# Performance work log

Measured on AMD Instinct MI355X. Metric: run time of the kernel, lower is better.

## Reference

```python
import jax, jax.numpy as jnp
import numpy as np

B, T, D = 2, 2048, 2048
H, KV, HD, RD = 16, 4, 128, 64  # n_heads, n_kv_heads, head_dim, rope_head_dim
THETA = 10000.0


def setup_inputs() -> dict:
    key = jax.random.key(0)
    ks = jax.random.split(key, 5)
    x = jax.random.normal(ks[0], (B, T, D), dtype=jnp.float32)
    Wq = jax.random.normal(ks[1], (D, H * HD), dtype=jnp.float32) * 0.02
    Wk = jax.random.normal(ks[2], (D, KV * HD), dtype=jnp.float32) * 0.02
    Wv = jax.random.normal(ks[3], (D, KV * HD), dtype=jnp.float32) * 0.02
    Wo = jax.random.normal(ks[4], (H * HD, D), dtype=jnp.float32) * 0.02
    # RoPE frequencies for the first RD dims of each head
    inv_freq = 1.0 / (THETA ** (jnp.arange(0, RD, 2, dtype=jnp.float32) / RD))  # [RD/2]
    ang = jnp.arange(T, dtype=jnp.float32)[:, None] * inv_freq[None, :]         # [T, RD/2]
    return {"x": x, "freqs_cos": jnp.cos(ang), "freqs_sin": jnp.sin(ang),
            "Wq": Wq, "Wk": Wk, "Wv": Wv, "Wo": Wo}


def _apply_rope(t, cos, sin):
    # t: [B, h, T, HD]; rotate first RD dims treating consecutive pairs as complex
    rot = t[..., :RD].reshape(*t.shape[:-1], RD // 2, 2)
    e, o = rot[..., 0], rot[..., 1]
    c = cos[None, None]  # [1,1,T,RD/2]
    s = sin[None, None]
    re = e * c - o * s
    ro = e * s + o * c
    rot_out = jnp.stack([re, ro], axis=-1).reshape(*t.shape[:-1], RD)
    return jnp.concatenate([rot_out, t[..., RD:]], axis=-1)


def reference(x, freqs_cos, freqs_sin, Wq, Wk, Wv, Wo):
    q = (x @ Wq).reshape(B, T, H, HD).transpose(0, 2, 1, 3)   # [B,H,T,HD]
    k = (x @ Wk).reshape(B, T, KV, HD).transpose(0, 2, 1, 3)  # [B,KV,T,HD]
    v = (x @ Wv).reshape(B, T, KV, HD).transpose(0, 2, 1, 3)
    q = _apply_rope(q, freqs_cos, freqs_sin)
    k = _apply_rope(k, freqs_cos, freqs_sin)
    present_k, present_v = k, v
    rep = H // KV
    kr = jnp.repeat(k, rep, axis=1)  # GQA repeat_interleave -> [B,H,T,HD]
    vr = jnp.repeat(v, rep, axis=1)
    scores = jnp.einsum('bhqd,bhkd->bhqk', q, kr) / jnp.sqrt(jnp.asarray(HD, q.dtype))
    causal = jnp.tril(jnp.ones((T, T), dtype=bool))
    scores = jnp.where(causal[None, None], scores, jnp.asarray(-1e9, scores.dtype))
    attn = jax.nn.softmax(scores, axis=-1)
    y = jnp.einsum('bhqk,bhkd->bhqd', attn, vr)
    y = y.transpose(0, 2, 1, 3).reshape(B, T, H * HD) @ Wo  # [B,T,D]
    return y, present_k, present_v
```

## Files before the change

kernel.cpp:

```cpp
#include <hip/hip_runtime.h>
#include <hip/hip_bf16.h>

static constexpr int B_  = 2;
static constexpr int T_  = 2048;
static constexpr int D_  = 2048;
static constexpr int H_  = 16;
static constexpr int KV_ = 4;
static constexpr int HD_ = 128;
static constexpr int RD_ = 64;
static constexpr int BT_ = B_ * T_;
static constexpr float SCALE_ = 0.08838834764831845f;

typedef __attribute__((ext_vector_type(8))) short bf16x8;
typedef __attribute__((ext_vector_type(8))) unsigned short u16x8;
typedef __attribute__((ext_vector_type(4))) float f32x4;

#define COMPILER_BARRIER() __asm__ __volatile__("" ::: "memory")

typedef const __attribute__((address_space(1))) unsigned int* as1_u32p;
typedef __attribute__((address_space(3))) unsigned int* as3_u32p;
#define GLOAD16(g, l) __builtin_amdgcn_global_load_lds((as1_u32p)(const void*)(g), (as3_u32p)(void*)(l), 16, 0, 0)

__device__ __forceinline__ unsigned short f2bu(float f) {
  unsigned x = __float_as_uint(f);
  unsigned r = (x + 0x7fffu + ((x >> 16) & 1u)) >> 16;
  return (unsigned short)r;
}

__global__ __launch_bounds__(256) void cvt_bf16(const float* __restrict__ in,
                                                unsigned short* __restrict__ out) {
  const size_t i = ((size_t)blockIdx.x * 256 + threadIdx.x) * 4;
  const float4 f = *(const float4*)(in + i);
  ushort4 o;
  o.x = f2bu(f.x); o.y = f2bu(f.y); o.z = f2bu(f.z); o.w = f2bu(f.w);
  *(ushort4*)(out + i) = o;
}

__global__ __launch_bounds__(256) void t32(const float* __restrict__ in,
                                           unsigned short* __restrict__ out,
                                           int R, int C) {
  __shared__ unsigned short tile[32][36];
  const int r0 = blockIdx.x * 32;
  const int c0 = blockIdx.y * 32;
  const int tid = threadIdx.x;
  {
    const int r = tid >> 3;
    const int c = (tid & 7) * 4;
    const float4 f = *(const float4*)(in + (size_t)(r0 + r) * C + c0 + c);
    ushort4 w;
    w.x = f2bu(f.x); w.y = f2bu(f.y); w.z = f2bu(f.z); w.w = f2bu(f.w);
    *(ushort4*)&tile[r][c] = w;
  }
  __syncthreads();
  {
    const int c = tid >> 3;
    const int r = (tid & 7) * 4;
    ushort4 o;
    o.x = tile[r + 0][c];
    o.y = tile[r + 1][c];
    o.z = tile[r + 2][c];
    o.w = tile[r + 3][c];
    *(ushort4*)(out + (size_t)(c0 + c) * R + r0 + r) = o;
  }
}

template <int REMAP>
__global__ __launch_bounds__(256) void gemm_bf16(const unsigned short* __restrict__ A,
                                                 const unsigned short* __restrict__ Bt,
                                                 float* __restrict__ C,
                                                 int M, int N, int K) {
  __shared__ __align__(16) unsigned short As[128 * 32];
  __shared__ __align__(16) unsigned short Bs[128 * 32];
  const int tid = threadIdx.x;
  const int lane = tid & 63;
  const int wave = tid >> 6;
  const int n16 = lane & 15;
  const int quad = lane >> 4;
  const int bm = blockIdx.y * 128;
  const int bn = blockIdx.x * 128;
  const int wm = (wave & 1) * 64;
  const int wn = (wave >> 1) * 64;

  const int gr = tid >> 2;
  const int gc = (tid & 3) * 8;
  const unsigned short* agA = A  + (size_t)(bm + gr) * K + gc;
  const unsigned short* agB = A  + (size_t)(bm + 64 + gr) * K + gc;
  const unsigned short* bgA = Bt + (size_t)(bn + gr) * K + gc;
  const unsigned short* bgB = Bt + (size_t)(bn + 64 + gr) * K + gc;
  unsigned short* lAs0 = As + wave * 512;
  unsigned short* lAs1 = As + 2048 + wave * 512;
  unsigned short* lBs0 = Bs + wave * 512;
  unsigned short* lBs1 = Bs + 2048 + wave * 512;

  f32x4 acc[4][4];
#pragma unroll
  for (int mi = 0; mi < 4; ++mi)
#pragma unroll
    for (int ni = 0; ni < 4; ++ni) acc[mi][ni] = (f32x4){0.f, 0.f, 0.f, 0.f};

  for (int k0 = 0; k0 < K; k0 += 32) {
    GLOAD16(agA + k0, lAs0);
    GLOAD16(agB + k0, lAs1);
    GLOAD16(bgA + k0, lBs0);
    GLOAD16(bgB + k0, lBs1);
    __syncthreads();

    bf16x8 af[4], bf[4];
#pragma unroll
    for (int i = 0; i < 4; ++i) {
      af[i] = *(const bf16x8*)&As[(wm + i * 16 + n16) * 32 + quad * 8];
      bf[i] = *(const bf16x8*)&Bs[(wn + i * 16 + n16) * 32 + quad * 8];
    }
#pragma unroll
    for (int mi = 0; mi < 4; ++mi)
#pragma unroll
      for (int ni = 0; ni < 4; ++ni)
        acc[mi][ni] = __builtin_amdgcn_mfma_f32_16x16x32_bf16(af[mi], bf[ni], acc[mi][ni], 0, 0, 0);
    __syncthreads();
  }

#pragma unroll
  for (int mi = 0; mi < 4; ++mi) {
#pragma unroll
    for (int r = 0; r < 4; ++r) {
      const int row = bm + wm + mi * 16 + quad * 4 + r;
#pragma unroll
      for (int ni = 0; ni < 4; ++ni) {
        const int col = bn + wn + ni * 16 + n16;
        const float v = acc[mi][ni][r];
        if (REMAP == 0) {
          C[(size_t)row * N + col] = v;
        } else {
          const int b = row >> 11, t = row & (T_ - 1);
          const int part = col >> 9;
          const int kv = (col >> 7) & 3;
          const int hd = col & 127;
          C[(size_t)part * (B_ * KV_ * T_ * HD_) +
            (((size_t)(b * KV_ + kv) * T_) + t) * HD_ + hd] = v;
        }
      }
    }
  }
}

__global__ __launch_bounds__(256) void rope_q(float* __restrict__ Q,
                                              const float* __restrict__ cosb,
                                              const float* __restrict__ sinb) {
  const int bt = blockIdx.x;
  const int t = bt % T_;
  const int tid = threadIdx.x;
  for (int i = tid; i < H_ * (RD_ / 2); i += 256) {
    const int h = i >> 5;
    const int p = i & 31;
    const float c = cosb[t * 32 + p];
    const float s = sinb[t * 32 + p];
    const size_t base = (size_t)bt * (H_ * HD_) + h * HD_ + 2 * p;
    const float e = Q[base], o = Q[base + 1];
    Q[base]     = e * c - o * s;
    Q[base + 1] = e * s + o * c;
  }
}

__global__ __launch_bounds__(256) void rope_k(float* __restrict__ kout,
                                              const float* __restrict__ cosb,
                                              const float* __restrict__ sinb,
                                              unsigned short* __restrict__ Kbf) {
  const int bt = blockIdx.x;
  const int t = bt % T_;
  const int b = bt / T_;
  const int tid = threadIdx.x;
  for (int i = tid; i < KV_ * (HD_ / 2); i += 256) {
    const int kv = i >> 6;
    const int p = i & 63;
    const size_t idx = (((size_t)(b * KV_ + kv) * T_) + t) * HD_ + 2 * p;
    float e = kout[idx], o = kout[idx + 1];
    if (p < 32) {
      const float c = cosb[t * 32 + p];
      const float s = sinb[t * 32 + p];
      const float re = e * c - o * s;
      const float ro = e * s + o * c;
      e = re; o = ro;
      kout[idx]     = e;
      kout[idx + 1] = o;
    }
    Kbf[idx]     = f2bu(e);
    Kbf[idx + 1] = f2bu(o);
  }
}

__global__ __launch_bounds__(256) void v_transpose(const float* __restrict__ vin,
                                                   unsigned short* __restrict__ vt) {
  __shared__ unsigned int tile[32][17];
  const int tid = threadIdx.x;
  const int k0 = blockIdx.x * 32;
  const int d0 = blockIdx.y * 32;
  const int g  = blockIdx.z;
  const float* src = vin + ((size_t)g * T_ + k0) * HD_ + d0;

  {
    const int kr = tid >> 3;
    const int d2 = (tid & 7) * 2;
#pragma unroll
    for (int c = 0; c < 2; ++c) {
      const float2 f = *(const float2*)(src + (size_t)kr * HD_ + (d2 + c) * 2);
      tile[kr][d2 + c] = (unsigned)f2bu(f.x) | ((unsigned)f2bu(f.y) << 16);
    }
  }
  __syncthreads();
  {
    const int dr = tid >> 3;
    const int kc = (tid & 7) * 4;
    const int dstb = ((kc & 15) << 1) | ((kc & 16) >> 2);
    const int hi = dr >> 1;
    const int sh = (dr & 1) * 16;
    ushort4 o;
    o.x = (unsigned short)(tile[kc + 0][hi] >> sh);
    o.y = (unsigned short)(tile[kc + 1][hi] >> sh);
    o.z = (unsigned short)(tile[kc + 2][hi] >> sh);
    o.w = (unsigned short)(tile[kc + 3][hi] >> sh);
    *(ushort4*)(vt + ((size_t)g * HD_ + d0 + dr) * T_ + k0 + dstb) = o;
  }
}

__global__ __launch_bounds__(256, 2) void attn_flash(const float* __restrict__ Q,
                                                     const unsigned short* __restrict__ Kbf,
                                                     const unsigned short* __restrict__ VbfT,
                                                     unsigned short* __restrict__ O) {
  __shared__ __align__(16) unsigned short Ks[32 * 128];
  __shared__ __align__(16) unsigned short Vs[128 * 32];
  __shared__ __align__(16) float mBr[4][16];
  __shared__ __align__(16) float mAr[4][16];
  __shared__ __align__(16) float lBr[4][16];
  __shared__ __align__(16) float lAr[4][16];

  const int tid = threadIdx.x;
  const int wave = tid >> 6;
  const int lane = tid & 63;
  const int n16 = lane & 15;
  const int quad = lane >> 4;
  const int pid = blockIdx.x;
  const int q0A = pid * 16;
  const int q0B = (127 - pid) * 16;
  const int nchA = (q0A + 47) >> 5;
  const int nchB = (q0B + 47) >> 5;
  const int bkv = blockIdx.y;
  const int b = bkv >> 2;
  const int kvh = bkv & 3;
  const int h = kvh * 4 + wave;

  const unsigned short* ksrc = Kbf + ((size_t)(b * KV_ + kvh)) * T_ * HD_;
  const unsigned short* vtsrc = VbfT + ((size_t)(b * KV_ + kvh)) * HD_ * T_;

  const int krow = tid >> 4;
  const int kcol = (tid & 15) * 8;
  const int kdst0 = (krow * 128 + kcol) ^ ((krow & 7) << 3);
  const int kdst1 = ((krow + 16) * 128 + kcol) ^ ((krow & 7) << 3);
  const int vrow = tid >> 2;
  const int vcol = (tid & 3) * 8;
  const int vdst0 = (vrow * 32 + vcol) ^ ((vrow & 3) << 3);
  const int vdst1 = ((vrow + 64) * 32 + vcol) ^ ((vrow & 3) << 3);

  bf16x8 qfA[4], qfB[4];
  {
    const float* qa = Q + ((size_t)(b * T_ + q0A + n16)) * (H_ * HD_) + h * HD_ + quad * 8;
    const float* qb = Q + ((size_t)(b * T_ + q0B + n16)) * (H_ * HD_) + h * HD_ + quad * 8;
#pragma unroll
    for (int s = 0; s < 4; ++s) {
      union { bf16x8 v; unsigned short u[8]; } ta, tb;
#pragma unroll
      for (int j = 0; j < 8; ++j) {
        ta.u[j] = f2bu(qa[s * 32 + j] * SCALE_);
        tb.u[j] = f2bu(qb[s * 32 + j] * SCALE_);
      }
      qfA[s] = ta.v; qfB[s] = tb.v;
    }
  }

  float mA = -1e30f, lA = 0.f;
  float mB = -1e30f, lB = 0.f;
  f32x4 oA[8], oB[8];
#pragma unroll
  for (int t = 0; t < 8; ++t) { oA[t] = (f32x4){0.f,0.f,0.f,0.f}; oB[t] = (f32x4){0.f,0.f,0.f,0.f}; }

  {
    const u16x8 ka = *(const u16x8*)(ksrc + (size_t)krow * HD_ + kcol);
    const u16x8 kb = *(const u16x8*)(ksrc + (size_t)(krow + 16) * HD_ + kcol);
    const u16x8 va = *(const u16x8*)(vtsrc + (size_t)vrow * T_ + vcol);
    const u16x8 vb = *(const u16x8*)(vtsrc + (size_t)(vrow + 64) * T_ + vcol);
    *(u16x8*)&Ks[kdst0] = ka;
    *(u16x8*)&Ks[kdst1] = kb;
    *(u16x8*)&Vs[vdst0] = va;
    *(u16x8*)&Vs[vdst1] = vb;
  }
  __syncthreads();

  for (int c = 0; c < nchB; ++c) {
    const int kc = c * 32;
    const bool actA = (c < nchA);

    u16x8 ka, kb, va, vb;
    if (c + 1 < nchB) {
      ka = *(const u16x8*)(ksrc + (size_t)(kc + 32 + krow) * HD_ + kcol);
      kb = *(const u16x8*)(ksrc + (size_t)(kc + 48 + krow) * HD_ + kcol);
      va = *(const u16x8*)(vtsrc + (size_t)vrow * T_ + (kc + 32) + vcol);
      vb = *(const u16x8*)(vtsrc + (size_t)(vrow + 64) * T_ + (kc + 32) + vcol);
    }
    COMPILER_BARRIER();

    f32x4 sB0 = (f32x4){0.f,0.f,0.f,0.f}, sB1 = sB0, sA0 = sB0, sA1 = sB0;
#pragma unroll
    for (int s = 0; s < 4; ++s) {
      const bf16x8 kf0 = *(const bf16x8*)&Ks[(n16 * 128 + quad * 8 + s * 32) ^ ((n16 & 7) << 3)];
      const bf16x8 kf1 = *(const bf16x8*)&Ks[((16 + n16) * 128 + quad * 8 + s * 32) ^ ((n16 & 7) << 3)];
      sB0 = __builtin_amdgcn_mfma_f32_16x16x32_bf16(kf0, qfB[s], sB0, 0, 0, 0);
      sB1 = __builtin_amdgcn_mfma_f32_16x16x32_bf16(kf1, qfB[s], sB1, 0, 0, 0);
      if (actA) {
        sA0 = __builtin_amdgcn_mfma_f32_16x16x32_bf16(kf0, qfA[s], sA0, 0, 0, 0);
        sA1 = __builtin_amdgcn_mfma_f32_16x16x32_bf16(kf1, qfA[s], sA1, 0, 0, 0);
      }
    }

    union { bf16x8 v; unsigned short u[8]; } pkB, pkA;
    bool growB;
    {
      float s[8];
#pragma unroll
      for (int r = 0; r < 4; ++r) { s[r] = sB0[r]; s[r + 4] = sB1[r]; }
      if (c == nchB - 1) {
        const int qrow = q0B + n16;
#pragma unroll
        for (int r = 0; r < 4; ++r) {
          if (kc + quad * 4 + r > qrow)      s[r]     = -1e30f;
          if (kc + 16 + quad * 4 + r > qrow) s[r + 4] = -1e30f;
        }
      }
      float mm = fmaxf(fmaxf(fmaxf(s[0], s[1]), fmaxf(s[2], s[3])),
                       fmaxf(fmaxf(s[4], s[5]), fmaxf(s[6], s[7])));
      mm = fmaxf(mm, __shfl_xor(mm, 16));
      mm = fmaxf(mm, __shfl_xor(mm, 32));
      growB = __any(mm > mB);
      float alpha = 1.f;
      if (growB) {
        const float mnew = fmaxf(mB, mm);
        alpha = __expf(mB - mnew);
        mB = mnew;
        if (quad == 0) mBr[wave][n16] = alpha;
      }
      float lsum = 0.f;
#pragma unroll
      for (int j = 0; j < 8; ++j) {
        const float p = __expf(s[j] - mB);
        lsum += p;
        pkB.u[j] = f2bu(p);
      }
      lsum += __shfl_xor(lsum, 16);
      lsum += __shfl_xor(lsum, 32);
      lB = growB ? (alpha * lB + lsum) : (lB + lsum);
    }

    bool growA = false;
    if (actA) {
      float s[8];
#pragma unroll
      for (int r = 0; r < 4; ++r) { s[r] = sA0[r]; s[r + 4] = sA1[r]; }
      if (c == nchA - 1) {
        const int qrow = q0A + n16;
#pragma unroll
        for (int r = 0; r < 4; ++r) {
          if (kc + quad * 4 + r > qrow)      s[r]     = -1e30f;
          if (kc + 16 + quad * 4 + r > qrow) s[r + 4] = -1e30f;
        }
      }
      float mm = fmaxf(fmaxf(fmaxf(s[0], s[1]), fmaxf(s[2], s[3])),
                       fmaxf(fmaxf(s[4], s[5]), fmaxf(s[6], s[7])));
      mm = fmaxf(mm, __shfl_xor(mm, 16));
      mm = fmaxf(mm, __shfl_xor(mm, 32));
      growA = __any(mm > mA);
      float alpha = 1.f;
      if (growA) {
        const float mnew = fmaxf(mA, mm);
        alpha = __expf(mA - mnew);
        mA = mnew;
        if (quad == 0) mAr[wave][n16] = alpha;
      }
      float lsum = 0.f;
#pragma unroll
      for (int j = 0; j < 8; ++j) {
        const float p = __expf(s[j] - mA);
        lsum += p;
        pkA.u[j] = f2bu(p);
      }
      lsum += __shfl_xor(lsum, 16);
      lsum += __shfl_xor(lsum, 32);
      lA = growA ? (alpha * lA + lsum) : (lA + lsum);
    }

    if (growB) {
      COMPILER_BARRIER();
      const f32x4 av = *(const f32x4*)&mBr[wave][quad * 4];
#pragma unroll
      for (int t = 0; t < 8; ++t) {
        oB[t][0] *= av[0]; oB[t][1] *= av[1]; oB[t][2] *= av[2]; oB[t][3] *= av[3];
      }
    }
    if (growA) {
      COMPILER_BARRIER();
      const f32x4 av = *(const f32x4*)&mAr[wave][quad * 4];
#pragma unroll
      for (int t = 0; t < 8; ++t) {
        oA[t][0] *= av[0]; oA[t][1] *= av[1]; oA[t][2] *= av[2]; oA[t][3] *= av[3];
      }
    }

#pragma unroll
    for (int t = 0; t < 8; ++t) {
      const bf16x8 vf = *(const bf16x8*)&Vs[((t * 16 + n16) * 32 + quad * 8) ^ ((n16 & 3) << 3)];
      oB[t] = __builtin_amdgcn_mfma_f32_16x16x32_bf16(pkB.v, vf, oB[t], 0, 0, 0);
      if (actA) oA[t] = __builtin_amdgcn_mfma_f32_16x16x32_bf16(pkA.v, vf, oA[t], 0, 0, 0);
    }

    __syncthreads();
    if (c + 1 < nchB) {
      *(u16x8*)&Ks[kdst0] = ka;
      *(u16x8*)&Ks[kdst1] = kb;
      *(u16x8*)&Vs[vdst0] = va;
      *(u16x8*)&Vs[vdst1] = vb;
    }
    __syncthreads();
  }

  if (quad == 0) { lBr[wave][n16] = lB; lAr[wave][n16] = lA; }
  COMPILER_BARRIER();
  {
    const f32x4 lBC = *(const f32x4*)&lBr[wave][quad * 4];
    const f32x4 lAC = *(const f32x4*)&lAr[wave][quad * 4];
    unsigned short* obB = O + ((size_t)(b * T_ + q0B)) * (H_ * HD_) + h * HD_;
    unsigned short* obA = O + ((size_t)(b * T_ + q0A)) * (H_ * HD_) + h * HD_;
#pragma unroll
    for (int r = 0; r < 4; ++r) {
      const float liB = 1.0f / lBC[r];
      const float liA = 1.0f / lAC[r];
#pragma unroll
      for (int t = 0; t < 8; ++t) {
        obB[(size_t)(quad * 4 + r) * (H_ * HD_) + t * 16 + n16] = f2bu(oB[t][r] * liB);
        obA[(size_t)(quad * 4 + r) * (H_ * HD_) + t * 16 + n16] = f2bu(oA[t][r] * liA);
      }
    }
  }
}

extern "C" void kernel_launch(void* const* d_in, const int* in_sizes, int n_in,
                              void* d_out, int out_size, void* d_ws, size_t ws_size,
                              hipStream_t stream) {
  const float* x  = (const float*)d_in[0];
  const float* fc = (const float*)d_in[1];
  const float* fs = (const float*)d_in[2];
  const float* Wq = (const float*)d_in[3];
  const float* Wk = (const float*)d_in[4];
  const float* Wv = (const float*)d_in[5];
  const float* Wo = (const float*)d_in[6];

  float* yout = (float*)d_out;
  float* kout = yout + (size_t)B_ * T_ * D_;
  float* vout = kout + (size_t)B_ * KV_ * T_ * HD_;
  float* Qb = yout;

  unsigned short* xb   = (unsigned short*)d_ws;
  unsigned short* Abf  = xb;
  unsigned short* Wqt  = xb   + (size_t)BT_ * D_;
  unsigned short* Wkvt = Wqt  + (size_t)D_ * D_;
  unsigned short* Wot  = Wkvt + (size_t)1024 * D_;
  unsigned short* Kbf  = Wot  + (size_t)D_ * D_;
  unsigned short* VbfT = Kbf  + (size_t)B_ * KV_ * T_ * HD_;

  dim3 blk(256);

  cvt_bf16<<<dim3((BT_ * D_) / 1024), blk, 0, stream>>>(x, xb);
  t32<<<dim3(D_ / 32, D_ / 32), blk, 0, stream>>>(Wq, Wqt, D_, D_);
  t32<<<dim3(D_ / 32, 512 / 32), blk, 0, stream>>>(Wk, Wkvt, D_, 512);
  t32<<<dim3(D_ / 32, 512 / 32), blk, 0, stream>>>(Wv, Wkvt + (size_t)512 * D_, D_, 512);
  t32<<<dim3(D_ / 32, D_ / 32), blk, 0, stream>>>(Wo, Wot, D_, D_);

  gemm_bf16<0><<<dim3(D_ / 128, BT_ / 128), blk, 0, stream>>>(xb, Wqt, Qb, BT_, D_, D_);
  gemm_bf16<1><<<dim3(1024 / 128, BT_ / 128), blk, 0, stream>>>(xb, Wkvt, kout, BT_, 1024, D_);

  rope_q<<<dim3(BT_), blk, 0, stream>>>(Qb, fc, fs);
  rope_k<<<dim3(BT_), blk, 0, stream>>>(kout, fc, fs, Kbf);
  v_transpose<<<dim3(T_ / 32, HD_ / 32, B_ * KV_), blk, 0, stream>>>(vout, VbfT);

  attn_flash<<<dim3(64, B_ * KV_), dim3(256), 0, stream>>>(Qb, Kbf, VbfT, Abf);

  gemm_bf16<0><<<dim3(D_ / 128, BT_ / 128), blk, 0, stream>>>(Abf, Wot, yout, BT_, D_, D_);
}
```

Baseline: 402.5 us.

## Fuse QKV projections with RoPE epilogue, merge weight transposes, store Q as bf16

Replaces the separate Q and KV projection GEMMs and both RoPE kernels with one GEMM over the concatenated 3072-column weight. Its epilogue applies RoPE using a lane shuffle for the pair partner, writes Q as pre-scaled bf16, and writes K in both fp32 and bf16 plus V. The four weight transposes become one launch, and attention loads bf16 Q directly. Attention also replaces LDS round-trips for the rescale factors and row sums with wave shuffles. This removes several launches and the fp32 Q round-trip through memory. The cost is a GEMM epilogue with branches and scattered per-element stores, and it relies on Wqt and Wkvt being laid out contiguously.

```diff
diff --git a/kernel.cpp b/kernel.cpp
--- a/kernel.cpp
+++ b/kernel.cpp
@@ -9,6 +9,7 @@
 static constexpr int HD_ = 128;
 static constexpr int RD_ = 64;
 static constexpr int BT_ = B_ * T_;
+static constexpr int NPROJ_ = 3072;
 static constexpr float SCALE_ = 0.08838834764831845f;
 
 typedef __attribute__((ext_vector_type(8))) short bf16x8;
@@ -36,9 +37,22 @@
   *(ushort4*)(out + i) = o;
 }
 
-__global__ __launch_bounds__(256) void t32(const float* __restrict__ in,
-                                           unsigned short* __restrict__ out,
-                                           int R, int C) {
+__global__ __launch_bounds__(256) void t32_all(const float* __restrict__ Wq,
+                                               const float* __restrict__ Wk,
+                                               const float* __restrict__ Wv,
+                                               const float* __restrict__ Wo,
+                                               unsigned short* __restrict__ Wqt,
+                                               unsigned short* __restrict__ Wkvt,
+                                               unsigned short* __restrict__ Wot) {
+  const float* in; unsigned short* out; int C;
+  switch (blockIdx.z) {
+    case 0:  in = Wq; out = Wqt;                       C = 2048; break;
+    case 1:  in = Wk; out = Wkvt;                      C = 512;  break;
+    case 2:  in = Wv; out = Wkvt + (size_t)512 * D_;   C = 512;  break;
+    default: in = Wo; out = Wot;                       C = 2048; break;
+  }
+  if ((int)blockIdx.y * 32 >= C) return;
+
   __shared__ unsigned short tile[32][36];
   const int r0 = blockIdx.x * 32;
   const int c0 = blockIdx.y * 32;
@@ -60,11 +74,103 @@
     o.y = tile[r + 1][c];
     o.z = tile[r + 2][c];
     o.w = tile[r + 3][c];
-    *(ushort4*)(out + (size_t)(c0 + c) * R + r0 + r) = o;
-  }
-}
-
-template <int REMAP>
+    *(ushort4*)(out + (size_t)(c0 + c) * D_ + r0 + r) = o;
+  }
+}
+
+__global__ __launch_bounds__(256) void gemm_proj(const unsigned short* __restrict__ A,
+                                                 const unsigned short* __restrict__ Bt,
+                                                 unsigned short* __restrict__ Qbf,
+                                                 float* __restrict__ kout,
+                                                 float* __restrict__ vout,
+                                                 unsigned short* __restrict__ Kbf,
+                                                 const float* __restrict__ cosb,
+                                                 const float* __restrict__ sinb) {
+  __shared__ __align__(16) unsigned short As[128 * 32];
+  __shared__ __align__(16) unsigned short Bs[128 * 32];
+  const int tid = threadIdx.x;
+  const int lane = tid & 63;
+  const int wave = tid >> 6;
+  const int n16 = lane & 15;
+  const int quad = lane >> 4;
+  const int bm = blockIdx.y * 128;
+  const int bn = blockIdx.x * 128;
+  const int wm = (wave & 1) * 64;
+  const int wn = (wave >> 1) * 64;
+  const int K = D_;
+
+  const int gr = tid >> 2;
+  const int gc = (tid & 3) * 8;
+  const unsigned short* agA = A  + (size_t)(bm + gr) * K + gc;
+  const unsigned short* agB = A  + (size_t)(bm + 64 + gr) * K + gc;
+  const unsigned short* bgA = Bt + (size_t)(bn + gr) * K + gc;
+  const unsigned short* bgB = Bt + (size_t)(bn + 64 + gr) * K + gc;
+  unsigned short* lAs0 = As + wave * 512;
+  unsigned short* lAs1 = As + 2048 + wave * 512;
+  unsigned short* lBs0 = Bs + wave * 512;
+  unsigned short* lBs1 = Bs + 2048 + wave * 512;
+
+  f32x4 acc[4][4];
+#pragma unroll
+  for (int mi = 0; mi < 4; ++mi)
+#pragma unroll
+    for (int ni = 0; ni < 4; ++ni) acc[mi][ni] = (f32x4){0.f, 0.f, 0.f, 0.f};
+
+  for (int k0 = 0; k0 < K; k0 += 32) {
+    GLOAD16(agA + k0, lAs0);
+    GLOAD16(agB + k0, lAs1);
+    GLOAD16(bgA + k0, lBs0);
+    GLOAD16(bgB + k0, lBs1);
+    __syncthreads();
+
+    bf16x8 af[4], bf[4];
+#pragma unroll
+    for (int i = 0; i < 4; ++i) {
+      af[i] = *(const bf16x8*)&As[(wm + i * 16 + n16) * 32 + quad * 8];
+      bf[i] = *(const bf16x8*)&Bs[(wn + i * 16 + n16) * 32 + quad * 8];
+    }
+#pragma unroll
+    for (int mi = 0; mi < 4; ++mi)
+#pragma unroll
+      for (int ni = 0; ni < 4; ++ni)
+        acc[mi][ni] = __builtin_amdgcn_mfma_f32_16x16x32_bf16(af[mi], bf[ni], acc[mi][ni], 0, 0, 0);
+    __syncthreads();
+  }
+
+  const int colbase = bn + wn;
+#pragma unroll
+  for (int mi = 0; mi < 4; ++mi) {
+#pragma unroll
+    for (int r = 0; r < 4; ++r) {
+      const int row = bm + wm + mi * 16 + quad * 4 + r;
+      const int b = row >> 11, t = row & (T_ - 1);
+#pragma unroll
+      for (int ni = 0; ni < 4; ++ni) {
+        const int col = colbase + ni * 16 + n16;
+        const int hd = col & 127;
+        float v = acc[mi][ni][r];
+        const float other = __shfl_xor(v, 1);
+        if (col < 2560 && hd < RD_) {
+          const float c = cosb[t * 32 + (hd >> 1)];
+          const float s = sinb[t * 32 + (hd >> 1)];
+          v = (col & 1) ? (other * s + v * c) : (v * c - other * s);
+        }
+        if (col < 2048) {
+          Qbf[(size_t)row * (H_ * HD_) + col] = f2bu(v * SCALE_);
+        } else if (col < 2560) {
+          const int kv = (col - 2048) >> 7;
+          const size_t idx = (((size_t)(b * KV_ + kv) * T_) + t) * HD_ + hd;
+          kout[idx] = v;
+          Kbf[idx] = f2bu(v);
+        } else {
+          const int kv = (col - 2560) >> 7;
+          vout[(((size_t)(b * KV_ + kv) * T_) + t) * HD_ + hd] = v;
+        }
+      }
+    }
+  }
+}
+
 __global__ __launch_bounds__(256) void gemm_bf16(const unsigned short* __restrict__ A,
                                                  const unsigned short* __restrict__ Bt,
                                                  float* __restrict__ C,
@@ -127,64 +233,9 @@
 #pragma unroll
       for (int ni = 0; ni < 4; ++ni) {
         const int col = bn + wn + ni * 16 + n16;
-        const float v = acc[mi][ni][r];
-        if (REMAP == 0) {
-          C[(size_t)row * N + col] = v;
-        } else {
-          const int b = row >> 11, t = row & (T_ - 1);
-          const int part = col >> 9;
-          const int kv = (col >> 7) & 3;
-          const int hd = col & 127;
-          C[(size_t)part * (B_ * KV_ * T_ * HD_) +
-            (((size_t)(b * KV_ + kv) * T_) + t) * HD_ + hd] = v;
-        }
-      }
-    }
-  }
-}
-
-__global__ __launch_bounds__(256) void rope_q(float* __restrict__ Q,
-                                              const float* __restrict__ cosb,
-                                              const float* __restrict__ sinb) {
-  const int bt = blockIdx.x;
-  const int t = bt % T_;
-  const int tid = threadIdx.x;
-  for (int i = tid; i < H_ * (RD_ / 2); i += 256) {
-    const int h = i >> 5;
-    const int p = i & 31;
-    const float c = cosb[t * 32 + p];
-    const float s = sinb[t * 32 + p];
-    const size_t base = (size_t)bt * (H_ * HD_) + h * HD_ + 2 * p;
-    const float e = Q[base], o = Q[base + 1];
-    Q[base]     = e * c - o * s;
-    Q[base + 1] = e * s + o * c;
-  }
-}
-
-__global__ __launch_bounds__(256) void rope_k(float* __restrict__ kout,
-                                              const float* __restrict__ cosb,
-                                              const float* __restrict__ sinb,
-                                              unsigned short* __restrict__ Kbf) {
-  const int bt = blockIdx.x;
-  const int t = bt % T_;
-  const int b = bt / T_;
-  const int tid = threadIdx.x;
-  for (int i = tid; i < KV_ * (HD_ / 2); i += 256) {
-    const int kv = i >> 6;
-    const int p = i & 63;
-    const size_t idx = (((size_t)(b * KV_ + kv) * T_) + t) * HD_ + 2 * p;
-    float e = kout[idx], o = kout[idx + 1];
-    if (p < 32) {
-      const float c = cosb[t * 32 + p];
-      const float s = sinb[t * 32 + p];
-      const float re = e * c - o * s;
-      const float ro = e * s + o * c;
-      e = re; o = ro;
-      kout[idx]     = e;
-      kout[idx + 1] = o;
-    }
-    Kbf[idx]     = f2bu(e);
-    Kbf[idx + 1] = f2bu(o);
+        C[(size_t)row * N + col] = acc[mi][ni][r];
+      }
+    }
   }
 }
 
@@ -222,16 +273,12 @@
   }
 }
 
-__global__ __launch_bounds__(256, 2) void attn_flash(const float* __restrict__ Q,
+__global__ __launch_bounds__(256, 2) void attn_flash(const unsigned short* __restrict__ Q,
                                                      const unsigned short* __restrict__ Kbf,
                                                      const unsigned short* __restrict__ VbfT,
                                                      unsigned short* __restrict__ O) {
   __shared__ __align__(16) unsigned short Ks[32 * 128];
   __shared__ __align__(16) unsigned short Vs[128 * 32];
-  __shared__ __align__(16) float mBr[4][16];
-  __shared__ __align__(16) float mAr[4][16];
-  __shared__ __align__(16) float lBr[4][16];
-  __shared__ __align__(16) float lAr[4][16];
 
   const int tid = threadIdx.x;
   const int wave = tid >> 6;
@@ -262,17 +309,12 @@
 
   bf16x8 qfA[4], qfB[4];
   {
-    const float* qa = Q + ((size_t)(b * T_ + q0A + n16)) * (H_ * HD_) + h * HD_ + quad * 8;
-    const float* qb = Q + ((size_t)(b * T_ + q0B + n16)) * (H_ * HD_) + h * HD_ + quad * 8;
+    const unsigned short* qa = Q + ((size_t)(b * T_ + q0A + n16)) * (H_ * HD_) + h * HD_ + quad * 8;
+    const unsigned short* qb = Q + ((size_t)(b * T_ + q0B + n16)) * (H_ * HD_) + h * HD_ + quad * 8;
 #pragma unroll
     for (int s = 0; s < 4; ++s) {
-      union { bf16x8 v; unsigned short u[8]; } ta, tb;
-#pragma unroll
-      for (int j = 0; j < 8; ++j) {
-        ta.u[j] = f2bu(qa[s * 32 + j] * SCALE_);
-        tb.u[j] = f2bu(qb[s * 32 + j] * SCALE_);
-      }
-      qfA[s] = ta.v; qfB[s] = tb.v;
+      qfA[s] = *(const bf16x8*)(qa + s * 32);
+      qfB[s] = *(const bf16x8*)(qb + s * 32);
     }
   }
 
@@ -322,6 +364,7 @@
 
     union { bf16x8 v; unsigned short u[8]; } pkB, pkA;
     bool growB;
+    float alphaB = 1.f, alphaA = 1.f;
     {
       float s[8];
 #pragma unroll
@@ -339,12 +382,10 @@
       mm = fmaxf(mm, __shfl_xor(mm, 16));
       mm = fmaxf(mm, __shfl_xor(mm, 32));
       growB = __any(mm > mB);
-      float alpha = 1.f;
       if (growB) {
         const float mnew = fmaxf(mB, mm);
-        alpha = __expf(mB - mnew);
+        alphaB = __expf(mB - mnew);
         mB = mnew;
-        if (quad == 0) mBr[wave][n16] = alpha;
       }
       float lsum = 0.f;
 #pragma unroll
@@ -355,7 +396,7 @@
       }
       lsum += __shfl_xor(lsum, 16);
       lsum += __shfl_xor(lsum, 32);
-      lB = growB ? (alpha * lB + lsum) : (lB + lsum);
+      lB = growB ? (alphaB * lB + lsum) : (lB + lsum);
     }
 
     bool growA = false;
@@ -376,12 +417,10 @@
       mm = fmaxf(mm, __shfl_xor(mm, 16));
       mm = fmaxf(mm, __shfl_xor(mm, 32));
       growA = __any(mm > mA);
-      float alpha = 1.f;
       if (growA) {
         const float mnew = fmaxf(mA, mm);
-        alpha = __expf(mA - mnew);
+        alphaA = __expf(mA - mnew);
         mA = mnew;
-        if (quad == 0) mAr[wave][n16] = alpha;
       }
       float lsum = 0.f;
 #pragma unroll
@@ -392,20 +431,22 @@
       }
       lsum += __shfl_xor(lsum, 16);
       lsum += __shfl_xor(lsum, 32);
-      lA = growA ? (alpha * lA + lsum) : (lA + lsum);
+      lA = growA ? (alphaA * lA + lsum) : (lA + lsum);
     }
 
     if (growB) {
-      COMPILER_BARRIER();
-      const f32x4 av = *(const f32x4*)&mBr[wave][quad * 4];
+      f32x4 av;
+#pragma unroll
+      for (int r = 0; r < 4; ++r) av[r] = __shfl(alphaB, quad * 4 + r);
 #pragma unroll
       for (int t = 0; t < 8; ++t) {
         oB[t][0] *= av[0]; oB[t][1] *= av[1]; oB[t][2] *= av[2]; oB[t][3] *= av[3];
       }
     }
     if (growA) {
-      COMPILER_BARRIER();
-      const f32x4 av = *(const f32x4*)&mAr[wave][quad * 4];
+      f32x4 av;
+#pragma unroll
+      for (int r = 0; r < 4; ++r) av[r] = __shfl(alphaA, quad * 4 + r);
 #pragma unroll
       for (int t = 0; t < 8; ++t) {
         oA[t][0] *= av[0]; oA[t][1] *= av[1]; oA[t][2] *= av[2]; oA[t][3] *= av[3];
@@ -429,17 +470,13 @@
     __syncthreads();
   }
 
-  if (quad == 0) { lBr[wave][n16] = lB; lAr[wave][n16] = lA; }
-  COMPILER_BARRIER();
-  {
-    const f32x4 lBC = *(const f32x4*)&lBr[wave][quad * 4];
-    const f32x4 lAC = *(const f32x4*)&lAr[wave][quad * 4];
+  {
     unsigned short* obB = O + ((size_t)(b * T_ + q0B)) * (H_ * HD_) + h * HD_;
     unsigned short* obA = O + ((size_t)(b * T_ + q0A)) * (H_ * HD_) + h * HD_;
 #pragma unroll
     for (int r = 0; r < 4; ++r) {
-      const float liB = 1.0f / lBC[r];
-      const float liA = 1.0f / lAC[r];
+      const float liB = 1.0f / __shfl(lB, quad * 4 + r);
+      const float liA = 1.0f / __shfl(lA, quad * 4 + r);
 #pragma unroll
       for (int t = 0; t < 8; ++t) {
         obB[(size_t)(quad * 4 + r) * (H_ * HD_) + t * 16 + n16] = f2bu(oB[t][r] * liB);
@@ -463,7 +500,7 @@
   float* yout = (float*)d_out;
   float* kout = yout + (size_t)B_ * T_ * D_;
   float* vout = kout + (size_t)B_ * KV_ * T_ * HD_;
-  float* Qb = yout;
+  unsigned short* Qbf = (unsigned short*)yout;
 
   unsigned short* xb   = (unsigned short*)d_ws;
   unsigned short* Abf  = xb;
@@ -476,19 +513,13 @@
   dim3 blk(256);
 
   cvt_bf16<<<dim3((BT_ * D_) / 1024), blk, 0, stream>>>(x, xb);
-  t32<<<dim3(D_ / 32, D_ / 32), blk, 0, stream>>>(Wq, Wqt, D_, D_);
-  t32<<<dim3(D_ / 32, 512 / 32), blk, 0, stream>>>(Wk, Wkvt, D_, 512);
-  t32<<<dim3(D_ / 32, 512 / 32), blk, 0, stream>>>(Wv, Wkvt + (size_t)512 * D_, D_, 512);
-  t32<<<dim3(D_ / 32, D_ / 32), blk, 0, stream>>>(Wo, Wot, D_, D_);
-
-  gemm_bf16<0><<<dim3(D_ / 128, BT_ / 128), blk, 0, stream>>>(xb, Wqt, Qb, BT_, D_, D_);
-  gemm_bf16<1><<<dim3(1024 / 128, BT_ / 128), blk, 0, stream>>>(xb, Wkvt, kout, BT_, 1024, D_);
-
-  rope_q<<<dim3(BT_), blk, 0, stream>>>(Qb, fc, fs);
-  rope_k<<<dim3(BT_), blk, 0, stream>>>(kout, fc, fs, Kbf);
+  t32_all<<<dim3(D_ / 32, D_ / 32, 4), blk, 0, stream>>>(Wq, Wk, Wv, Wo, Wqt, Wkvt, Wot);
+
+  gemm_proj<<<dim3(NPROJ_ / 128, BT_ / 128), blk, 0, stream>>>(xb, Wqt, Qbf, kout, vout, Kbf, fc, fs);
+
   v_transpose<<<dim3(T_ / 32, HD_ / 32, B_ * KV_), blk, 0, stream>>>(vout, VbfT);
 
-  attn_flash<<<dim3(64, B_ * KV_), dim3(256), 0, stream>>>(Qb, Kbf, VbfT, Abf);
-
-  gemm_bf16<0><<<dim3(D_ / 128, BT_ / 128), blk, 0, stream>>>(Abf, Wot, yout, BT_, D_, D_);
-}
+  attn_flash<<<dim3(64, B_ * KV_), blk, 0, stream>>>(Qbf, Kbf, VbfT, Abf);
+
+  gemm_bf16<<<dim3(D_ / 128, BT_ / 128), blk, 0, stream>>>(Abf, Wot, yout, BT_, D_, D_);
+}
```

Measured after the change: 405.2 us. No clear change (+0.7%).
